# Kernel tuning notes

Measured on AMD Instinct MI355X. Metric: run time of the kernel, lower is better.

The kernel has to match this reference:

```python
import jax, jax.numpy as jnp
import numpy as np

NUM_LEVELS = 3
NUM_EMBEDDINGS = 1024
EMBEDDING_DIM = 128
COMMITMENT_COST = 0.25
N_TOKENS = 262144


def setup_inputs() -> dict:
    key = jax.random.key(0)
    k1, k2 = jax.random.split(key)
    z_e = jax.random.normal(k1, (N_TOKENS, EMBEDDING_DIM), dtype=jnp.float32)
    codebooks = jax.random.normal(k2, (NUM_LEVELS, NUM_EMBEDDINGS, EMBEDDING_DIM), dtype=jnp.float32)
    return {"z_e": z_e, "codebooks": codebooks}


def _rvq_forward(z_e, codebooks):
    """Sequential residual VQ: per level cdist + argmin + gather + residual update.

    Per-level losses follow the standard EMA-VQ formulation:
      vq_loss     = mean((z_q - sg(residual))^2)
      commit_loss = beta * mean((sg(z_q) - residual)^2)
    with straight-through estimator z_q_st = residual + sg(z_q - residual).
    """
    sg = jax.lax.stop_gradient
    residual = z_e
    z_q_total = jnp.zeros_like(z_e)
    all_indices = []
    vq_loss = jnp.float32(0.0)
    commit_loss = jnp.float32(0.0)
    num_levels = codebooks.shape[0]
    for lvl in range(num_levels):  # small fixed loop over levels (sequential by design)
        E = codebooks[lvl]  # [K, D]
        # squared-distance matrix [N, K]: ||r||^2 + ||e||^2 - 2 r.e
        d = (jnp.sum(residual * residual, axis=1, keepdims=True)
             + jnp.sum(E * E, axis=1)
             - 2.0 * (residual @ E.T))
        idx = jnp.argmin(d, axis=1)           # [N]
        z_q = E[idx]                           # gather [N, D]
        vq_loss = vq_loss + jnp.mean((z_q - sg(residual)) ** 2)
        commit_loss = commit_loss + COMMITMENT_COST * jnp.mean((sg(z_q) - residual) ** 2)
        z_q_st = residual + sg(z_q - residual)  # straight-through
        z_q_total = z_q_total + z_q_st
        residual = residual - z_q_st
        all_indices.append(idx)
    L = jnp.float32(num_levels)
    stacked_indices = jnp.stack(all_indices, axis=1)  # [N, num_levels]
    return z_q_total, vq_loss / L, commit_loss / L, stacked_indices


def reference(z_e, codebooks):
    return _rvq_forward(z_e, codebooks)
```

## Files before the change

kernel.cpp:

```cpp
#include <hip/hip_runtime.h>
#include <math.h>

#define N_TOK   262144
#define DIMV    128
#define KCODE   1024
#define LEV     3
#define BLOCK   256
#define NTILES  64
#define EPS     0.08f

typedef _Float16 f16x8 __attribute__((ext_vector_type(8)));
typedef float f32x4 __attribute__((ext_vector_type(4)));


__global__ void rvq_prep(const float* __restrict__ cb, double* __restrict__ ws) {
    int c = blockIdx.x * blockDim.x + threadIdx.x;
    if (c == 0) ws[0] = 0.0;
    if (c < LEV * KCODE) {
        const float* e = cb + (size_t)c * DIMV;
        double s = 0.0;
        #pragma unroll 8
        for (int j = 0; j < DIMV; ++j) { double v = (double)e[j]; s = fma(v, v, s); }
        ws[8 + c] = s;
        ((float*)(ws + 8 + LEV * KCODE))[c] = (float)(s + 8192.0);
    }
}

__device__ inline void stage_write(unsigned char* dst, int woff, float4 g0, float4 g1) {
    f16x8 v;
    v[0]=(_Float16)g0.x; v[1]=(_Float16)g0.y; v[2]=(_Float16)g0.z; v[3]=(_Float16)g0.w;
    v[4]=(_Float16)g1.x; v[5]=(_Float16)g1.y; v[6]=(_Float16)g1.z; v[7]=(_Float16)g1.w;
    *(f16x8*)(dst + woff) = v;
}

__device__ inline unsigned sel4(const unsigned v[4], int j) {
    unsigned a = (j & 1) ? v[1] : v[0];
    unsigned b = (j & 1) ? v[3] : v[2];
    return (j & 2) ? b : a;
}

__global__ __launch_bounds__(BLOCK, 2) void rvq_main(const float* __restrict__ ze,
                                                     const float* __restrict__ cb,
                                                     float* __restrict__ out,
                                                     double* __restrict__ ws) {
    __shared__ __align__(16) unsigned char Bbuf[2][4096];
    __shared__ __align__(16) float eeS[KCODE];
    __shared__ double ssum[4];

    const double* __restrict__ ee64g = ws + 8;
    const float*  __restrict__ eebg  = (const float*)(ws + 8 + LEV * KCODE);

    const int tid  = threadIdx.x;
    const int lane = tid & 63;
    const int wid  = tid >> 6;
    const int q    = lane >> 4;
    const int col  = lane & 15;
    const long tokbase = (long)blockIdx.x * 128 + wid * 32;

    const int wc   = (((tid >> 2) & 3) << 6) | ((tid & 3) << 4) | (tid >> 4);
    const int woff = (wc ^ ((wc >> 4) & 7)) << 4;
    const int ro_e = (lane ^ (lane >> 4)) << 4;
    const int ro_o = (lane ^ 4 ^ (lane >> 4)) << 4;

    float r[2][4][8];
    f16x8 Ah[2][4], Al[2][4];

    #pragma unroll
    for (int mt = 0; mt < 2; ++mt) {
        const float4* zp = (const float4*)(ze + (size_t)(tokbase + mt*16 + col) * DIMV);
        #pragma unroll
        for (int st = 0; st < 4; ++st) {
            float4 a = zp[st*8 + q*2], b = zp[st*8 + q*2 + 1];
            r[mt][st][0]=a.x; r[mt][st][1]=a.y; r[mt][st][2]=a.z; r[mt][st][3]=a.w;
            r[mt][st][4]=b.x; r[mt][st][5]=b.y; r[mt][st][6]=b.z; r[mt][st][7]=b.w;
        }
    }
    #pragma unroll
    for (int mt = 0; mt < 2; ++mt)
        #pragma unroll
        for (int st = 0; st < 4; ++st) {
            f16x8 h, lo;
            #pragma unroll
            for (int j = 0; j < 8; ++j) {
                float x = r[mt][st][j];
                _Float16 hh = (_Float16)x;
                h[j] = hh;
                lo[j] = (_Float16)(x - (float)hh);
            }
            Ah[mt][st] = h; Al[mt][st] = lo;
        }

    double loss = 0.0;
    float* out_idx = out + (size_t)N_TOK * DIMV + 2;

    for (int l = 0; l < LEV; ++l) {
        __syncthreads();
        ((float4*)eeS)[tid] = ((const float4*)(eebg + (size_t)l * KCODE))[tid];
        float4 g0, g1;
        {
            const float4* p = (const float4*)(cb + ((size_t)l*KCODE + (tid>>4)) * DIMV + (tid&15)*8);
            g0 = p[0]; g1 = p[1];
            stage_write(Bbuf[0], woff, g0, g1);
        }
        __syncthreads();

        unsigned m1[2][4], m2[2][4];
        #pragma unroll
        for (int mt = 0; mt < 2; ++mt)
            #pragma unroll
            for (int i = 0; i < 4; ++i) { m1[mt][i] = 0xFFFFFFFFu; m2[mt][i] = 0xFFFFFFFFu; }

        for (int t = 0; t < NTILES; ++t) {
            if (t < NTILES - 1) {
                const float4* p = (const float4*)(cb + ((size_t)l*KCODE + (t+1)*16 + (tid>>4)) * DIMV + (tid&15)*8);
                g0 = p[0]; g1 = p[1];
            }
            {
                const unsigned char* bb = Bbuf[t & 1];
                f16x8 B0 = *(const f16x8*)(bb + ro_e);
                f16x8 B1 = *(const f16x8*)(bb + 1024 + ro_o);
                f16x8 B2 = *(const f16x8*)(bb + 2048 + ro_e);
                f16x8 B3 = *(const f16x8*)(bb + 3072 + ro_o);
                float eeq = eeS[t*16 + col];
                f32x4 c0 = {0.f,0.f,0.f,0.f}, c1v = {0.f,0.f,0.f,0.f};
                c0  = __builtin_amdgcn_mfma_f32_16x16x32_f16(Ah[0][0], B0, c0, 0,0,0);
                c0  = __builtin_amdgcn_mfma_f32_16x16x32_f16(Al[0][0], B0, c0, 0,0,0);
                c1v = __builtin_amdgcn_mfma_f32_16x16x32_f16(Ah[1][0], B0, c1v, 0,0,0);
                c1v = __builtin_amdgcn_mfma_f32_16x16x32_f16(Al[1][0], B0, c1v, 0,0,0);
                c0  = __builtin_amdgcn_mfma_f32_16x16x32_f16(Ah[0][1], B1, c0, 0,0,0);
                c0  = __builtin_amdgcn_mfma_f32_16x16x32_f16(Al[0][1], B1, c0, 0,0,0);
                c1v = __builtin_amdgcn_mfma_f32_16x16x32_f16(Ah[1][1], B1, c1v, 0,0,0);
                c1v = __builtin_amdgcn_mfma_f32_16x16x32_f16(Al[1][1], B1, c1v, 0,0,0);
                c0  = __builtin_amdgcn_mfma_f32_16x16x32_f16(Ah[0][2], B2, c0, 0,0,0);
                c0  = __builtin_amdgcn_mfma_f32_16x16x32_f16(Al[0][2], B2, c0, 0,0,0);
                c1v = __builtin_amdgcn_mfma_f32_16x16x32_f16(Ah[1][2], B2, c1v, 0,0,0);
                c1v = __builtin_amdgcn_mfma_f32_16x16x32_f16(Al[1][2], B2, c1v, 0,0,0);
                c0  = __builtin_amdgcn_mfma_f32_16x16x32_f16(Ah[0][3], B3, c0, 0,0,0);
                c0  = __builtin_amdgcn_mfma_f32_16x16x32_f16(Al[0][3], B3, c0, 0,0,0);
                c1v = __builtin_amdgcn_mfma_f32_16x16x32_f16(Ah[1][3], B3, c1v, 0,0,0);
                c1v = __builtin_amdgcn_mfma_f32_16x16x32_f16(Al[1][3], B3, c1v, 0,0,0);
                #pragma unroll
                for (int i = 0; i < 4; ++i) {
                    unsigned k0 = (__float_as_uint(fmaf(-2.0f, c0[i],  eeq)) << 6) | (unsigned)t;
                    m2[0][i] = min(m2[0][i], max(m1[0][i], k0));
                    m1[0][i] = min(m1[0][i], k0);
                    unsigned k1_ = (__float_as_uint(fmaf(-2.0f, c1v[i], eeq)) << 6) | (unsigned)t;
                    m2[1][i] = min(m2[1][i], max(m1[1][i], k1_));
                    m1[1][i] = min(m1[1][i], k1_);
                }
            }
            if (t < NTILES - 1) stage_write(Bbuf[(t+1)&1], woff, g0, g1);
            __syncthreads();
        }

        unsigned k1[2][4], k2[2][4], q1[2][4], q2[2][4];
        #pragma unroll
        for (int mt = 0; mt < 2; ++mt)
            #pragma unroll
            for (int i = 0; i < 4; ++i) {
                k1[mt][i] = m1[mt][i]; k2[mt][i] = m2[mt][i];
                q1[mt][i] = (unsigned)col; q2[mt][i] = (unsigned)col;
            }
        #pragma unroll
        for (int d = 1; d <= 8; d <<= 1) {
            #pragma unroll
            for (int mt = 0; mt < 2; ++mt)
                #pragma unroll
                for (int i = 0; i < 4; ++i) {
                    unsigned ok1 = __shfl_xor(k1[mt][i], d), oq1 = __shfl_xor(q1[mt][i], d);
                    unsigned ok2 = __shfl_xor(k2[mt][i], d), oq2 = __shfl_xor(q2[mt][i], d);
                    bool sw = (ok1 < k1[mt][i]) || (ok1 == k1[mt][i] && oq1 < q1[mt][i]);
                    unsigned n1 = sw ? ok1 : k1[mt][i], nq1 = sw ? oq1 : q1[mt][i];
                    unsigned hk = sw ? k1[mt][i] : ok1, hq = sw ? q1[mt][i] : oq1;
                    bool s2 = (ok2 < k2[mt][i]) || (ok2 == k2[mt][i] && oq2 < q2[mt][i]);
                    unsigned p2 = s2 ? ok2 : k2[mt][i], pq = s2 ? oq2 : q2[mt][i];
                    bool s3 = (p2 < hk) || (p2 == hk && pq < hq);
                    k1[mt][i] = n1;              q1[mt][i] = nq1;
                    k2[mt][i] = s3 ? p2 : hk;    q2[mt][i] = s3 ? pq : hq;
                }
        }

        int jsel = (lane >> 2) & 3;
        int S = ((col >> 2) << 4) | ((col & 3) << 2);

        #pragma unroll
        for (int mt = 0; mt < 2; ++mt) {
            unsigned sk1 = sel4(k1[mt], jsel), sq1 = sel4(q1[mt], jsel);
            unsigned sk2 = sel4(k2[mt], jsel), sq2 = sel4(q2[mt], jsel);
            unsigned bk1 = (unsigned)__shfl((int)sk1, S);
            unsigned bq1 = (unsigned)__shfl((int)sq1, S);
            unsigned bk2 = (unsigned)__shfl((int)sk2, S);
            unsigned bq2 = (unsigned)__shfl((int)sq2, S);
            int c1c = (int)(((bk1 & 63u) << 4) | bq1);
            int c2c = (int)(((bk2 & 63u) << 4) | bq2);
            float d1 = __uint_as_float((bk1 >> 6) | 0x44000000u) - 8192.0f;
            float d2 = __uint_as_float((bk2 >> 6) | 0x44000000u) - 8192.0f;
            int bc = c1c;
            if (d2 - d1 < EPS) {
                double s1 = 0.0, s2d = 0.0;
                const float4* e1 = (const float4*)(cb + ((size_t)l*KCODE + c1c)*DIMV);
                const float4* e2 = (const float4*)(cb + ((size_t)l*KCODE + c2c)*DIMV);
                #pragma unroll
                for (int st = 0; st < 4; ++st) {
                    float4 a = e1[st*8 + q*2], b = e1[st*8 + q*2 + 1];
                    s1 = fma((double)a.x,(double)r[mt][st][0],s1); s1 = fma((double)a.y,(double)r[mt][st][1],s1);
                    s1 = fma((double)a.z,(double)r[mt][st][2],s1); s1 = fma((double)a.w,(double)r[mt][st][3],s1);
                    s1 = fma((double)b.x,(double)r[mt][st][4],s1); s1 = fma((double)b.y,(double)r[mt][st][5],s1);
                    s1 = fma((double)b.z,(double)r[mt][st][6],s1); s1 = fma((double)b.w,(double)r[mt][st][7],s1);
                    float4 a2 = e2[st*8 + q*2], b2 = e2[st*8 + q*2 + 1];
                    s2d = fma((double)a2.x,(double)r[mt][st][0],s2d); s2d = fma((double)a2.y,(double)r[mt][st][1],s2d);
                    s2d = fma((double)a2.z,(double)r[mt][st][2],s2d); s2d = fma((double)a2.w,(double)r[mt][st][3],s2d);
                    s2d = fma((double)b2.x,(double)r[mt][st][4],s2d); s2d = fma((double)b2.y,(double)r[mt][st][5],s2d);
                    s2d = fma((double)b2.z,(double)r[mt][st][6],s2d); s2d = fma((double)b2.w,(double)r[mt][st][7],s2d);
                }
                s1  += __shfl_xor(s1, 16);  s1  += __shfl_xor(s1, 32);
                s2d += __shfl_xor(s2d, 16); s2d += __shfl_xor(s2d, 32);
                double dd1 = ee64g[l*KCODE + c1c] - 2.0*s1;
                double dd2 = ee64g[l*KCODE + c2c] - 2.0*s2d;
                if (dd2 < dd1 || (dd2 == dd1 && c2c < c1c)) bc = c2c;
            }
            const float4* eb = (const float4*)(cb + ((size_t)l*KCODE + bc)*DIMV);
            #pragma unroll
            for (int st = 0; st < 4; ++st) {
                float4 a = eb[st*8 + q*2], b = eb[st*8 + q*2 + 1];
                float qv[8] = {a.x,a.y,a.z,a.w,b.x,b.y,b.z,b.w};
                #pragma unroll
                for (int j = 0; j < 8; ++j) {
                    float rv = r[mt][st][j];
                    float t1 = qv[j] - rv;
                    loss += (double)t1 * (double)t1;
                    float zqst = rv + t1;
                    r[mt][st][j] = rv - zqst;
                }
            }
            if (l < LEV - 1) {
                #pragma unroll
                for (int st = 0; st < 4; ++st) {
                    f16x8 h, lo;
                    #pragma unroll
                    for (int j = 0; j < 8; ++j) {
                        float x = r[mt][st][j];
                        _Float16 hh = (_Float16)x;
                        h[j] = hh;
                        lo[j] = (_Float16)(x - (float)hh);
                    }
                    Ah[mt][st] = h; Al[mt][st] = lo;
                }
            } else {
                const float4* zp = (const float4*)(ze + (size_t)(tokbase + mt*16 + col)*DIMV);
                float4* op = (float4*)(out + (size_t)(tokbase + mt*16 + col)*DIMV);
                #pragma unroll
                for (int st = 0; st < 4; ++st) {
                    float4 za = zp[st*8 + q*2], zb = zp[st*8 + q*2 + 1];
                    float4 oa, ob;
                    oa.x = za.x - r[mt][st][0]; oa.y = za.y - r[mt][st][1];
                    oa.z = za.z - r[mt][st][2]; oa.w = za.w - r[mt][st][3];
                    ob.x = zb.x - r[mt][st][4]; ob.y = zb.y - r[mt][st][5];
                    ob.z = zb.z - r[mt][st][6]; ob.w = zb.w - r[mt][st][7];
                    op[st*8 + q*2] = oa; op[st*8 + q*2 + 1] = ob;
                }
            }
            if (q == 0) out_idx[(size_t)(tokbase + mt*16 + col)*3 + l] = (float)bc;
        }
    }

    #pragma unroll
    for (int d = 1; d <= 32; d <<= 1) loss += __shfl_xor(loss, d);
    if ((tid & 63) == 0) ssum[wid] = loss;
    __syncthreads();
    if (tid == 0) atomicAdd(ws, ssum[0] + ssum[1] + ssum[2] + ssum[3]);
}

__global__ void rvq_fin(const double* __restrict__ ws, float* __restrict__ out) {
    double vq = ws[0] / ((double)N_TOK * (double)DIMV * (double)LEV);
    out[(size_t)N_TOK * DIMV + 0] = (float)vq;
    out[(size_t)N_TOK * DIMV + 1] = (float)(0.25 * vq);
}

extern "C" void kernel_launch(void* const* d_in, const int* in_sizes, int n_in,
                              void* d_out, int out_size, void* d_ws, size_t ws_size,
                              hipStream_t stream) {
    const float* ze = (const float*)d_in[0];
    const float* cb = (const float*)d_in[1];
    float* out = (float*)d_out;
    double* ws = (double*)d_ws;

    rvq_prep<<<(LEV * KCODE + 255) / 256, 256, 0, stream>>>(cb, ws);
    rvq_main<<<N_TOK / 128, BLOCK, 0, stream>>>(ze, cb, out, ws);
    rvq_fin<<<1, 1, 0, stream>>>(ws, out);
}
```

Baseline: 762.6 us.

## Deepen codebook staging ring and fold distance bias into MFMA accumulator

Grows the shared-memory codebook ring from 2 to 8 tiles, prefetching 4 tiles ahead, so one barrier covers four tiles instead of one. The -2 scale is folded into the split-fp16 residual operands and the MFMA accumulators are seeded with ||e||^2, which removes the per-element FMA from the argmin loop. MFMA calls are interleaved across the two accumulators to hide their dependency latency. The cost is 32KB of LDS per block, which may lower occupancy. Pre-scaling by -2 is exact in fp16, so the hi/lo split keeps its precision.

```diff
diff --git a/kernel.cpp b/kernel.cpp
--- a/kernel.cpp
+++ b/kernel.cpp
@@ -43,7 +43,7 @@
                                                      const float* __restrict__ cb,
                                                      float* __restrict__ out,
                                                      double* __restrict__ ws) {
-    __shared__ __align__(16) unsigned char Bbuf[2][4096];
+    __shared__ __align__(16) unsigned char Bbuf[8][4096];
     __shared__ __align__(16) float eeS[KCODE];
     __shared__ double ssum[4];
 
@@ -82,10 +82,10 @@
             f16x8 h, lo;
             #pragma unroll
             for (int j = 0; j < 8; ++j) {
-                float x = r[mt][st][j];
-                _Float16 hh = (_Float16)x;
+                float y = -2.0f * r[mt][st][j];
+                _Float16 hh = (_Float16)y;
                 h[j] = hh;
-                lo[j] = (_Float16)(x - (float)hh);
+                lo[j] = (_Float16)(y - (float)hh);
             }
             Ah[mt][st] = h; Al[mt][st] = lo;
         }
@@ -96,60 +96,68 @@
     for (int l = 0; l < LEV; ++l) {
         __syncthreads();
         ((float4*)eeS)[tid] = ((const float4*)(eebg + (size_t)l * KCODE))[tid];
-        float4 g0, g1;
         {
             const float4* p = (const float4*)(cb + ((size_t)l*KCODE + (tid>>4)) * DIMV + (tid&15)*8);
-            g0 = p[0]; g1 = p[1];
-            stage_write(Bbuf[0], woff, g0, g1);
+            #pragma unroll
+            for (int i = 0; i < 4; ++i) {
+                stage_write(Bbuf[i], woff, p[0], p[1]);
+                p += 512;
+            }
         }
         __syncthreads();
 
+        const float4* pp = (const float4*)(cb + ((size_t)l*KCODE + 64 + (tid>>4)) * DIMV + (tid&15)*8);
+
         unsigned m1[2][4], m2[2][4];
         #pragma unroll
         for (int mt = 0; mt < 2; ++mt)
             #pragma unroll
             for (int i = 0; i < 4; ++i) { m1[mt][i] = 0xFFFFFFFFu; m2[mt][i] = 0xFFFFFFFFu; }
 
-        for (int t = 0; t < NTILES; ++t) {
-            if (t < NTILES - 1) {
-                const float4* p = (const float4*)(cb + ((size_t)l*KCODE + (t+1)*16 + (tid>>4)) * DIMV + (tid&15)*8);
-                g0 = p[0]; g1 = p[1];
-            }
-            {
-                const unsigned char* bb = Bbuf[t & 1];
-                f16x8 B0 = *(const f16x8*)(bb + ro_e);
-                f16x8 B1 = *(const f16x8*)(bb + 1024 + ro_o);
-                f16x8 B2 = *(const f16x8*)(bb + 2048 + ro_e);
-                f16x8 B3 = *(const f16x8*)(bb + 3072 + ro_o);
-                float eeq = eeS[t*16 + col];
-                f32x4 c0 = {0.f,0.f,0.f,0.f}, c1v = {0.f,0.f,0.f,0.f};
-                c0  = __builtin_amdgcn_mfma_f32_16x16x32_f16(Ah[0][0], B0, c0, 0,0,0);
-                c0  = __builtin_amdgcn_mfma_f32_16x16x32_f16(Al[0][0], B0, c0, 0,0,0);
-                c1v = __builtin_amdgcn_mfma_f32_16x16x32_f16(Ah[1][0], B0, c1v, 0,0,0);
-                c1v = __builtin_amdgcn_mfma_f32_16x16x32_f16(Al[1][0], B0, c1v, 0,0,0);
-                c0  = __builtin_amdgcn_mfma_f32_16x16x32_f16(Ah[0][1], B1, c0, 0,0,0);
-                c0  = __builtin_amdgcn_mfma_f32_16x16x32_f16(Al[0][1], B1, c0, 0,0,0);
-                c1v = __builtin_amdgcn_mfma_f32_16x16x32_f16(Ah[1][1], B1, c1v, 0,0,0);
-                c1v = __builtin_amdgcn_mfma_f32_16x16x32_f16(Al[1][1], B1, c1v, 0,0,0);
-                c0  = __builtin_amdgcn_mfma_f32_16x16x32_f16(Ah[0][2], B2, c0, 0,0,0);
-                c0  = __builtin_amdgcn_mfma_f32_16x16x32_f16(Al[0][2], B2, c0, 0,0,0);
-                c1v = __builtin_amdgcn_mfma_f32_16x16x32_f16(Ah[1][2], B2, c1v, 0,0,0);
-                c1v = __builtin_amdgcn_mfma_f32_16x16x32_f16(Al[1][2], B2, c1v, 0,0,0);
-                c0  = __builtin_amdgcn_mfma_f32_16x16x32_f16(Ah[0][3], B3, c0, 0,0,0);
-                c0  = __builtin_amdgcn_mfma_f32_16x16x32_f16(Al[0][3], B3, c0, 0,0,0);
-                c1v = __builtin_amdgcn_mfma_f32_16x16x32_f16(Ah[1][3], B3, c1v, 0,0,0);
-                c1v = __builtin_amdgcn_mfma_f32_16x16x32_f16(Al[1][3], B3, c1v, 0,0,0);
-                #pragma unroll
-                for (int i = 0; i < 4; ++i) {
-                    unsigned k0 = (__float_as_uint(fmaf(-2.0f, c0[i],  eeq)) << 6) | (unsigned)t;
-                    m2[0][i] = min(m2[0][i], max(m1[0][i], k0));
-                    m1[0][i] = min(m1[0][i], k0);
-                    unsigned k1_ = (__float_as_uint(fmaf(-2.0f, c1v[i], eeq)) << 6) | (unsigned)t;
-                    m2[1][i] = min(m2[1][i], max(m1[1][i], k1_));
-                    m1[1][i] = min(m1[1][i], k1_);
-                }
-            }
-            if (t < NTILES - 1) stage_write(Bbuf[(t+1)&1], woff, g0, g1);
+        for (int tb = 0; tb < NTILES; tb += 4) {
+            const int pre = (tb + 4 < NTILES);
+            #pragma unroll
+            for (int s = 0; s < 4; ++s) {
+                const int t = tb + s;
+                float4 g0, g1;
+                if (pre) { g0 = pp[0]; g1 = pp[1]; pp += 512; }
+                {
+                    const unsigned char* bb = Bbuf[t & 7];
+                    f16x8 B0 = *(const f16x8*)(bb + ro_e);
+                    f16x8 B1 = *(const f16x8*)(bb + 1024 + ro_o);
+                    f16x8 B2 = *(const f16x8*)(bb + 2048 + ro_e);
+                    f16x8 B3 = *(const f16x8*)(bb + 3072 + ro_o);
+                    float eeq = eeS[t*16 + col];
+                    f32x4 c0  = {eeq, eeq, eeq, eeq};
+                    f32x4 c1v = {eeq, eeq, eeq, eeq};
+                    c0  = __builtin_amdgcn_mfma_f32_16x16x32_f16(Ah[0][0], B0, c0, 0,0,0);
+                    c1v = __builtin_amdgcn_mfma_f32_16x16x32_f16(Ah[1][0], B0, c1v, 0,0,0);
+                    c0  = __builtin_amdgcn_mfma_f32_16x16x32_f16(Al[0][0], B0, c0, 0,0,0);
+                    c1v = __builtin_amdgcn_mfma_f32_16x16x32_f16(Al[1][0], B0, c1v, 0,0,0);
+                    c0  = __builtin_amdgcn_mfma_f32_16x16x32_f16(Ah[0][1], B1, c0, 0,0,0);
+                    c1v = __builtin_amdgcn_mfma_f32_16x16x32_f16(Ah[1][1], B1, c1v, 0,0,0);
+                    c0  = __builtin_amdgcn_mfma_f32_16x16x32_f16(Al[0][1], B1, c0, 0,0,0);
+                    c1v = __builtin_amdgcn_mfma_f32_16x16x32_f16(Al[1][1], B1, c1v, 0,0,0);
+                    c0  = __builtin_amdgcn_mfma_f32_16x16x32_f16(Ah[0][2], B2, c0, 0,0,0);
+                    c1v = __builtin_amdgcn_mfma_f32_16x16x32_f16(Ah[1][2], B2, c1v, 0,0,0);
+                    c0  = __builtin_amdgcn_mfma_f32_16x16x32_f16(Al[0][2], B2, c0, 0,0,0);
+                    c1v = __builtin_amdgcn_mfma_f32_16x16x32_f16(Al[1][2], B2, c1v, 0,0,0);
+                    c0  = __builtin_amdgcn_mfma_f32_16x16x32_f16(Ah[0][3], B3, c0, 0,0,0);
+                    c1v = __builtin_amdgcn_mfma_f32_16x16x32_f16(Ah[1][3], B3, c1v, 0,0,0);
+                    c0  = __builtin_amdgcn_mfma_f32_16x16x32_f16(Al[0][3], B3, c0, 0,0,0);
+                    c1v = __builtin_amdgcn_mfma_f32_16x16x32_f16(Al[1][3], B3, c1v, 0,0,0);
+                    #pragma unroll
+                    for (int i = 0; i < 4; ++i) {
+                        unsigned k0 = (__float_as_uint(c0[i]) << 6) | (unsigned)t;
+                        m2[0][i] = min(m2[0][i], max(m1[0][i], k0));
+                        m1[0][i] = min(m1[0][i], k0);
+                        unsigned k1_ = (__float_as_uint(c1v[i]) << 6) | (unsigned)t;
+                        m2[1][i] = min(m2[1][i], max(m1[1][i], k1_));
+                        m1[1][i] = min(m1[1][i], k1_);
+                    }
+                }
+                if (pre) stage_write(Bbuf[(t+4)&7], woff, g0, g1);
+            }
             __syncthreads();
         }
 
@@ -239,10 +247,10 @@
                     f16x8 h, lo;
                     #pragma unroll
                     for (int j = 0; j < 8; ++j) {
-                        float x = r[mt][st][j];
-                        _Float16 hh = (_Float16)x;
+                        float y = -2.0f * r[mt][st][j];
+                        _Float16 hh = (_Float16)y;
                         h[j] = hh;
-                        lo[j] = (_Float16)(x - (float)hh);
+                        lo[j] = (_Float16)(y - (float)hh);
                     }
                     Ah[mt][st] = h; Al[mt][st] = lo;
                 }
```

Result: faster. 708.4 us (-7.1%).
